# Kernel tuning notes

Hardware: AMD Instinct MI355X
Metric: run time of the kernel (lower is better)

## Reference

```python
import jax, jax.numpy as jnp
import numpy as np

NH = 12   # num_heads
EPS = 1e-6


def _layer_norm(x):
    m = jnp.mean(x, axis=-1, keepdims=True)
    v = jnp.mean((x - m) ** 2, axis=-1, keepdims=True)
    return (x - m) * jax.lax.rsqrt(v + EPS)


def _rms_norm(x, w):
    return x * jax.lax.rsqrt(jnp.mean(x * x, axis=-1, keepdims=True) + EPS) * w


def _rope_cos_sin(f, h, w, head_dim):
    # matches rope_params + calculate_freqs_i: split c=head_dim//2 complex freqs
    # into [c-2*(c//3), c//3, c//3] for the (F,H,W) axes.
    c = head_dim // 2
    inv = 1.0 / (10000.0 ** (np.arange(0, head_dim, 2, dtype=np.float64) / head_dim))
    c1 = c - 2 * (c // 3); c2 = c // 3
    af = np.outer(np.arange(f), inv[:c1])
    ah = np.outer(np.arange(h), inv[c1:c1 + c2])
    aw = np.outer(np.arange(w), inv[c1 + c2:])
    ang = np.concatenate([
        np.broadcast_to(af[:, None, None, :], (f, h, w, c1)),
        np.broadcast_to(ah[None, :, None, :], (f, h, w, c2)),
        np.broadcast_to(aw[None, None, :, :], (f, h, w, c2)),
    ], axis=-1).reshape(f * h * w, c)
    return jnp.asarray(np.cos(ang), jnp.float32), jnp.asarray(np.sin(ang), jnp.float32)


def _apply_rope(x, cos, sin):
    # complex rotation on interleaved pairs; x: [B,L,n,d]
    B, L, n, d = x.shape
    xr = x.reshape(B, L, n, d // 2, 2)
    x0, x1 = xr[..., 0], xr[..., 1]
    co = cos[None, :, None, :]; si = sin[None, :, None, :]
    return jnp.stack([x0 * co - x1 * si, x0 * si + x1 * co], axis=-1).reshape(B, L, n, d)


def _attention(q, k, v):
    scale = 1.0 / jnp.sqrt(jnp.asarray(q.shape[-1], q.dtype))
    s = jnp.einsum('blnd,bmnd->bnlm', q, k) * scale
    return jnp.einsum('bnlm,bmnd->blnd', jax.nn.softmax(s, axis=-1), v)


def _block(x, e, context, mod, sa_wq, sa_bq, sa_wk, sa_bk, sa_wv, sa_bv, sa_wo, sa_bo,
           sa_nq, sa_nk, n3_w, n3_b, ca_wq, ca_bq, ca_wk, ca_bk, ca_wv, ca_bv, ca_wo,
           ca_bo, ca_nq, ca_nk, ffn_w1, ffn_b1, ffn_w2, ffn_b2, f, h, w):
    B, L, C = x.shape
    D = C // NH
    em = mod + e                      # [B,6,C] AdaLN shift/scale/gate params
    cos, sin = _rope_cos_sin(f, h, w, D)
    # --- self-attention with AdaLN modulation + RoPE + qk RMSNorm ---
    xa = _layer_norm(x) * (1.0 + em[:, 1:2]) + em[:, 0:1]
    q = _rms_norm(xa @ sa_wq + sa_bq, sa_nq).reshape(B, L, NH, D)
    k = _rms_norm(xa @ sa_wk + sa_bk, sa_nk).reshape(B, L, NH, D)
    v = (xa @ sa_wv + sa_bv).reshape(B, L, NH, D)
    q = _apply_rope(q, cos, sin)
    k = _apply_rope(k, cos, sin)
    y = _attention(q, k, v).reshape(B, L, C) @ sa_wo + sa_bo
    x = x + y * em[:, 2:3]
    # --- t2v cross-attention (norm3 is affine LayerNorm) ---
    L2 = context.shape[1]
    xc = _layer_norm(x) * n3_w + n3_b
    q = _rms_norm(xc @ ca_wq + ca_bq, ca_nq).reshape(B, L, NH, D)
    k = _rms_norm(context @ ca_wk + ca_bk, ca_nk).reshape(B, L2, NH, D)
    v = (context @ ca_wv + ca_bv).reshape(B, L2, NH, D)
    x = x + (_attention(q, k, v).reshape(B, L, C) @ ca_wo + ca_bo)
    # --- FFN (GELU-tanh) with AdaLN modulation ---
    xf = _layer_norm(x) * (1.0 + em[:, 4:5]) + em[:, 3:4]
    y = jax.nn.gelu(xf @ ffn_w1 + ffn_b1, approximate=True) @ ffn_w2 + ffn_b2
    return x + y * em[:, 5:6]


def setup_inputs() -> dict:
    key = jax.random.key(0)
    ks = jax.random.split(key, 16)
    B, L2, C, FFN = 1, 512, 1536, 8960
    F, H, W = 9, 16, 28
    L = F * H * W  # 4032
    def mk(i, shape, s=0.02):
        return jax.random.normal(ks[i], shape, jnp.float32) * s
    return {
        'x': jax.random.normal(ks[0], (B, L, C), jnp.float32),
        'e': jax.random.normal(ks[1], (B, 6, C), jnp.float32),
        'context': jax.random.normal(ks[2], (B, L2, C), jnp.float32),
        'mod': jax.random.normal(ks[3], (1, 6, C), jnp.float32) / jnp.sqrt(float(C)),
        'sa_wq': mk(4, (C, C)), 'sa_bq': jnp.zeros((C,), jnp.float32),
        'sa_wk': mk(5, (C, C)), 'sa_bk': jnp.zeros((C,), jnp.float32),
        'sa_wv': mk(6, (C, C)), 'sa_bv': jnp.zeros((C,), jnp.float32),
        'sa_wo': mk(7, (C, C)), 'sa_bo': jnp.zeros((C,), jnp.float32),
        'sa_nq': jnp.ones((C,), jnp.float32), 'sa_nk': jnp.ones((C,), jnp.float32),
        'n3_w': jnp.ones((C,), jnp.float32), 'n3_b': jnp.zeros((C,), jnp.float32),
        'ca_wq': mk(8, (C, C)), 'ca_bq': jnp.zeros((C,), jnp.float32),
        'ca_wk': mk(9, (C, C)), 'ca_bk': jnp.zeros((C,), jnp.float32),
        'ca_wv': mk(10, (C, C)), 'ca_bv': jnp.zeros((C,), jnp.float32),
        'ca_wo': mk(11, (C, C)), 'ca_bo': jnp.zeros((C,), jnp.float32),
        'ca_nq': jnp.ones((C,), jnp.float32), 'ca_nk': jnp.ones((C,), jnp.float32),
        'ffn_w1': mk(12, (C, FFN)), 'ffn_b1': jnp.zeros((FFN,), jnp.float32),
        'ffn_w2': mk(13, (FFN, C)), 'ffn_b2': jnp.zeros((C,), jnp.float32),
        'f': F, 'h': H, 'w': W,
    }


def reference(x, e, context, mod, sa_wq, sa_bq, sa_wk, sa_bk, sa_wv, sa_bv, sa_wo,
              sa_bo, sa_nq, sa_nk, n3_w, n3_b, ca_wq, ca_bq, ca_wk, ca_bk, ca_wv,
              ca_bv, ca_wo, ca_bo, ca_nq, ca_nk, ffn_w1, ffn_b1, ffn_w2, ffn_b2,
              f, h, w):
    return _block(x, e, context, mod, sa_wq, sa_bq, sa_wk, sa_bk, sa_wv, sa_bv,
                  sa_wo, sa_bo, sa_nq, sa_nk, n3_w, n3_b, ca_wq, ca_bq, ca_wk,
                  ca_bk, ca_wv, ca_bv, ca_wo, ca_bo, ca_nq, ca_nk, ffn_w1, ffn_b1,
                  ffn_w2, ffn_b2, f, h, w)
```

## Files before the change

### kernel.cpp

```cpp
#include <hip/hip_runtime.h>
#include <math.h>


#define L_SEQ 4032
#define L_PAD 4096
#define C_DIM 1536
#define L_CTX 512
#define FFN_DIM 8960
#define NHEAD 12
#define DHEAD 128

typedef __attribute__((ext_vector_type(8))) short short8;
typedef __attribute__((ext_vector_type(4))) float floatx4;

__device__ inline unsigned short f2bf(float x) {
  unsigned int u = __float_as_uint(x);
  u += 0x7fffu + ((u >> 16) & 1u);
  return (unsigned short)(u >> 16);
}

__device__ inline float2 block_sum2(float2 v) {
  __shared__ float2 red[4];
#pragma unroll
  for (int o = 32; o > 0; o >>= 1) {
    v.x += __shfl_xor(v.x, o, 64);
    v.y += __shfl_xor(v.y, o, 64);
  }
  int wave = threadIdx.x >> 6;
  if ((threadIdx.x & 63) == 0) red[wave] = v;
  __syncthreads();
  float2 t = make_float2(0.f, 0.f);
#pragma unroll
  for (int i = 0; i < 4; ++i) { t.x += red[i].x; t.y += red[i].y; }
  return t;
}

__global__ void add_kernel(float* __restrict__ o, const float* __restrict__ a,
                           const float* __restrict__ b, int n) {
  int i = blockIdx.x * 256 + threadIdx.x;
  if (i < n) o[i] = a[i] + b[i];
}

__global__ void concat3_kernel(float* __restrict__ o, const float* __restrict__ a,
                               const float* __restrict__ b, const float* __restrict__ c) {
  int i = blockIdx.x * 256 + threadIdx.x;
  if (i < C_DIM) {
    o[i] = a[i];
    o[C_DIM + i] = b[i];
    if (c) o[2 * C_DIM + i] = c[i];
  }
}

__global__ void f32_to_bf16_kernel(unsigned short* __restrict__ o,
                                   const float* __restrict__ in, int n) {
  int i = (blockIdx.x * 256 + threadIdx.x) * 4;
  if (i < n) {
    float4 v = *(const float4*)&in[i];
    ushort4 o4 = {f2bf(v.x), f2bf(v.y), f2bf(v.z), f2bf(v.w)};
    *(ushort4*)&o[i] = o4;
  }
}

__global__ __launch_bounds__(256) void transpose_bf16_kernel(
    const float* __restrict__ W, unsigned short* __restrict__ WT, int K, int N) {
  __shared__ float t[32][33];
  int n0 = blockIdx.x * 32, k0 = blockIdx.y * 32;
  int c = threadIdx.x & 31, r0 = threadIdx.x >> 5;
#pragma unroll
  for (int i = 0; i < 4; ++i) {
    int r = r0 + 8 * i;
    t[r][c] = W[(size_t)(k0 + r) * N + n0 + c];
  }
  __syncthreads();
#pragma unroll
  for (int i = 0; i < 4; ++i) {
    int r = r0 + 8 * i;
    WT[(size_t)(n0 + r) * K + k0 + c] = f2bf(t[c][r]);
  }
}

__global__ __launch_bounds__(256) void transpose_v_kernel(
    const float* __restrict__ V, unsigned short* __restrict__ Vt, int stride, int Lk) {
  __shared__ float t[32][33];
  int k0 = blockIdx.x * 32, c0 = blockIdx.y * 32;
  int c = threadIdx.x & 31, r0 = threadIdx.x >> 5;
#pragma unroll
  for (int i = 0; i < 4; ++i) {
    int r = r0 + 8 * i;
    t[r][c] = V[(size_t)(k0 + r) * stride + c0 + c];
  }
  __syncthreads();
#pragma unroll
  for (int i = 0; i < 4; ++i) {
    int r = r0 + 8 * i;
    Vt[(size_t)(c0 + r) * Lk + k0 + c] = f2bf(t[c][r]);
  }
}

__global__ __launch_bounds__(256) void ln_affine_kernel(
    unsigned short* __restrict__ out, const float* __restrict__ in,
    const float* __restrict__ sc, const float* __restrict__ sh, float addOne) {
  int row = blockIdx.x;
  const float* xr = in + (size_t)row * C_DIM;
  float vals[C_DIM / 256];
  float2 p = make_float2(0.f, 0.f);
  int cnt = 0;
  for (int c = threadIdx.x; c < C_DIM; c += 256) {
    float v = xr[c];
    vals[cnt++] = v;
    p.x += v; p.y += v * v;
  }
  float2 t = block_sum2(p);
  float mean = t.x * (1.f / C_DIM);
  float var = t.y * (1.f / C_DIM) - mean * mean;
  float r = rsqrtf(var + 1e-6f);
  cnt = 0;
  for (int c = threadIdx.x; c < C_DIM; c += 256) {
    float xh = (vals[cnt++] - mean) * r;
    out[(size_t)row * C_DIM + c] = f2bf(xh * (addOne + sc[c]) + sh[c]);
  }
}

template <int ROPE>
__global__ __launch_bounds__(256) void rms_post_kernel(
    unsigned short* __restrict__ obf, const float* __restrict__ in,
    const float* __restrict__ w, const float* __restrict__ cosb,
    const float* __restrict__ sinb, int stride, float ps) {
  int row = blockIdx.x;
  const float* xr = in + (size_t)row * stride;
  int c0 = threadIdx.x * 6;
  float v[6];
  *(float2*)&v[0] = *(const float2*)&xr[c0];
  *(float2*)&v[2] = *(const float2*)&xr[c0 + 2];
  *(float2*)&v[4] = *(const float2*)&xr[c0 + 4];
  float s2 = 0.f;
#pragma unroll
  for (int i = 0; i < 6; ++i) s2 += v[i] * v[i];
  float2 t = block_sum2(make_float2(s2, 0.f));
  float r = rsqrtf(t.x * (1.f / C_DIM) + 1e-6f) * ps;
#pragma unroll
  for (int i = 0; i < 6; ++i) v[i] *= r * w[c0 + i];
  if (ROPE) {
#pragma unroll
    for (int i = 0; i < 3; ++i) {
      int c = c0 + 2 * i;
      int j = (c & 127) >> 1;
      float co = cosb[row * 64 + j], si = sinb[row * 64 + j];
      float a = v[2 * i], b = v[2 * i + 1];
      v[2 * i] = a * co - b * si;
      v[2 * i + 1] = a * si + b * co;
    }
  }
  unsigned short* op = obf + (size_t)row * C_DIM + c0;
  ushort2 o01 = {f2bf(v[0]), f2bf(v[1])};
  ushort2 o23 = {f2bf(v[2]), f2bf(v[3])};
  ushort2 o45 = {f2bf(v[4]), f2bf(v[5])};
  *(ushort2*)&op[0] = o01;
  *(ushort2*)&op[2] = o23;
  *(ushort2*)&op[4] = o45;
}

__global__ void rope_tables_kernel(float* __restrict__ cosb, float* __restrict__ sinb) {
  int l = blockIdx.x, j = threadIdx.x;
  int f = l / (16 * 28);
  int rem = l % (16 * 28);
  int hh = rem / 28, ww = rem % 28;
  double inv = pow(10000.0, -(double)(2 * j) / 128.0);
  double pos = (j < 22) ? (double)f : ((j < 43) ? (double)hh : (double)ww);
  double ang = pos * inv;
  cosb[l * 64 + j] = (float)cos(ang);
  sinb[l * 64 + j] = (float)sin(ang);
}

__device__ inline float gelu_tanh(float x) {
  float x3 = x * x * x;
  return 0.5f * x * (1.f + tanhf(0.79788456080286535588f * (x + 0.044715f * x3)));
}

__device__ inline int xcd_remap(int flat, int nwg) {
  int qq = nwg >> 3, rr = nwg & 7;
  int xcd = flat & 7, idx = flat >> 3;
  return (xcd < rr ? xcd * (qq + 1) : rr * (qq + 1) + (xcd - rr) * qq) + idx;
}

template <int EPI>
__global__ __launch_bounds__(256) void mgemm_kernel(
    const unsigned short* __restrict__ A, const unsigned short* __restrict__ BT,
    const float* __restrict__ bias, void* __restrict__ Cout,
    const float* __restrict__ resid, const float* __restrict__ gate,
    int N, int K, int Mlimit) {
  __shared__ short sA[3][4096];
  __shared__ short sB[3][4096];
  const int tid = threadIdx.x;
  const int wv = tid >> 6, lane = tid & 63;
  const int lm = lane & 15, lq = lane >> 4;
  const int wr = wv >> 1, wc = wv & 1;

  const int gx = gridDim.x;
  int flat = xcd_remap(blockIdx.y * gx + blockIdx.x, gx * gridDim.y);
  const int row0 = (flat / gx) * 128, col0 = (flat % gx) * 128;

  floatx4 zero4 = {0.f, 0.f, 0.f, 0.f};
  floatx4 acc[4][4];
#pragma unroll
  for (int i = 0; i < 4; ++i)
#pragma unroll
    for (int j = 0; j < 4; ++j) acc[i][j] = zero4;

  const unsigned short* Abase = A + ((size_t)row0 + lm) * K + lq * 8;
  const unsigned short* Bbase = BT + ((size_t)col0 + lm) * K + lq * 8;

  auto stage = [&](int buf, int k0) {
#pragma unroll
    for (int t = 0; t < 2; ++t) {
      int g = wv * 2 + t;
      __builtin_amdgcn_global_load_lds(
          (const __attribute__((address_space(1))) void*)(Abase + (size_t)(g * 16) * K + k0),
          (__attribute__((address_space(3))) void*)(sA[buf] + g * 512), 16, 0, 0);
      __builtin_amdgcn_global_load_lds(
          (const __attribute__((address_space(1))) void*)(Bbase + (size_t)(g * 16) * K + k0),
          (__attribute__((address_space(3))) void*)(sB[buf] + g * 512), 16, 0, 0);
    }
  };

  stage(0, 0);
  stage(1, 32);
  asm volatile("s_waitcnt vmcnt(4)" ::: "memory");
  __builtin_amdgcn_s_barrier();
  __builtin_amdgcn_sched_barrier(0);

  int cur = 0;
  const int nk = K >> 5;
  for (int t = 0; t < nk; ++t) {
    int b2 = cur + 2; if (b2 >= 3) b2 -= 3;
    const bool more = (t + 2 < nk);
    if (more) stage(b2, (t + 2) << 5);
    const short* sAc = &sA[cur][0];
    const short* sBc = &sB[cur][0];
    short8 af[4], bfv[4];
#pragma unroll
    for (int mt = 0; mt < 4; ++mt)
      af[mt] = *(const short8*)(sAc + (wr * 4 + mt) * 512 + lane * 8);
#pragma unroll
    for (int nt = 0; nt < 4; ++nt)
      bfv[nt] = *(const short8*)(sBc + (wc * 4 + nt) * 512 + lane * 8);
#pragma unroll
    for (int mt = 0; mt < 4; ++mt)
#pragma unroll
      for (int nt = 0; nt < 4; ++nt)
        acc[mt][nt] = __builtin_amdgcn_mfma_f32_16x16x32_bf16(
            af[mt], bfv[nt], acc[mt][nt], 0, 0, 0);
    __builtin_amdgcn_sched_barrier(0);
    if (more) { asm volatile("s_waitcnt vmcnt(4)" ::: "memory"); }
    else      { asm volatile("s_waitcnt vmcnt(0)" ::: "memory"); }
    __builtin_amdgcn_s_barrier();
    __builtin_amdgcn_sched_barrier(0);
    cur = (cur + 1 == 3) ? 0 : cur + 1;
  }

#pragma unroll
  for (int nt = 0; nt < 4; ++nt) {
    int colg = col0 + wc * 64 + nt * 16 + lm;
    float bv = bias[colg];
    float gv = (EPI == 2 && gate) ? gate[colg] : 1.f;
#pragma unroll
    for (int mt = 0; mt < 4; ++mt) {
#pragma unroll
      for (int r = 0; r < 4; ++r) {
        int rowg = row0 + wr * 64 + mt * 16 + lq * 4 + r;
        if (rowg < Mlimit) {
          float v = acc[mt][nt][r] + bv;
          if (EPI == 1) {
            ((unsigned short*)Cout)[(size_t)rowg * N + colg] = f2bf(gelu_tanh(v));
          } else if (EPI == 2) {
            ((float*)Cout)[(size_t)rowg * N + colg] =
                resid[(size_t)rowg * N + colg] + v * gv;
          } else {
            ((float*)Cout)[(size_t)rowg * N + colg] = v;
          }
        }
      }
    }
  }
}

template <int EPI>
__global__ __launch_bounds__(256) void mgemm64_kernel(
    const unsigned short* __restrict__ A, const unsigned short* __restrict__ BT,
    const float* __restrict__ bias, void* __restrict__ Cout,
    const float* __restrict__ resid, const float* __restrict__ gate,
    int N, int K, int Mlimit) {
  __shared__ short sA[3][2048];
  __shared__ short sB[3][4096];
  const int tid = threadIdx.x;
  const int wv = tid >> 6, lane = tid & 63;
  const int lm = lane & 15, lq = lane >> 4;
  const int wc = wv;

  const int gx = gridDim.x;
  int flat = xcd_remap(blockIdx.y * gx + blockIdx.x, gx * gridDim.y);
  const int row0 = (flat / gx) * 64, col0 = (flat % gx) * 128;

  floatx4 zero4 = {0.f, 0.f, 0.f, 0.f};
  floatx4 acc[4][2];
#pragma unroll
  for (int i = 0; i < 4; ++i)
#pragma unroll
    for (int j = 0; j < 2; ++j) acc[i][j] = zero4;

  const unsigned short* Abase = A + ((size_t)row0 + lm) * K + lq * 8;
  const unsigned short* Bbase = BT + ((size_t)col0 + lm) * K + lq * 8;

  auto stage = [&](int buf, int k0) {
    __builtin_amdgcn_global_load_lds(
        (const __attribute__((address_space(1))) void*)(Abase + (size_t)(wv * 16) * K + k0),
        (__attribute__((address_space(3))) void*)(sA[buf] + wv * 512), 16, 0, 0);
#pragma unroll
    for (int t = 0; t < 2; ++t) {
      int g = wv * 2 + t;
      __builtin_amdgcn_global_load_lds(
          (const __attribute__((address_space(1))) void*)(Bbase + (size_t)(g * 16) * K + k0),
          (__attribute__((address_space(3))) void*)(sB[buf] + g * 512), 16, 0, 0);
    }
  };

  stage(0, 0);
  stage(1, 32);
  asm volatile("s_waitcnt vmcnt(3)" ::: "memory");
  __builtin_amdgcn_s_barrier();
  __builtin_amdgcn_sched_barrier(0);

  int cur = 0;
  const int nk = K >> 5;
  for (int t = 0; t < nk; ++t) {
    int b2 = cur + 2; if (b2 >= 3) b2 -= 3;
    const bool more = (t + 2 < nk);
    if (more) stage(b2, (t + 2) << 5);
    const short* sAc = &sA[cur][0];
    const short* sBc = &sB[cur][0];
    short8 af[4], bfv[2];
#pragma unroll
    for (int mt = 0; mt < 4; ++mt)
      af[mt] = *(const short8*)(sAc + mt * 512 + lane * 8);
#pragma unroll
    for (int nt = 0; nt < 2; ++nt)
      bfv[nt] = *(const short8*)(sBc + (wc * 2 + nt) * 512 + lane * 8);
#pragma unroll
    for (int mt = 0; mt < 4; ++mt)
#pragma unroll
      for (int nt = 0; nt < 2; ++nt)
        acc[mt][nt] = __builtin_amdgcn_mfma_f32_16x16x32_bf16(
            af[mt], bfv[nt], acc[mt][nt], 0, 0, 0);
    __builtin_amdgcn_sched_barrier(0);
    if (more) { asm volatile("s_waitcnt vmcnt(3)" ::: "memory"); }
    else      { asm volatile("s_waitcnt vmcnt(0)" ::: "memory"); }
    __builtin_amdgcn_s_barrier();
    __builtin_amdgcn_sched_barrier(0);
    cur = (cur + 1 == 3) ? 0 : cur + 1;
  }

#pragma unroll
  for (int nt = 0; nt < 2; ++nt) {
    int colg = col0 + wc * 32 + nt * 16 + lm;
    float bv = bias[colg];
    float gv = (EPI == 2 && gate) ? gate[colg] : 1.f;
#pragma unroll
    for (int mt = 0; mt < 4; ++mt) {
#pragma unroll
      for (int r = 0; r < 4; ++r) {
        int rowg = row0 + mt * 16 + lq * 4 + r;
        if (rowg < Mlimit) {
          float v = acc[mt][nt][r] + bv;
          if (EPI == 1) {
            ((unsigned short*)Cout)[(size_t)rowg * N + colg] = f2bf(gelu_tanh(v));
          } else if (EPI == 2) {
            ((float*)Cout)[(size_t)rowg * N + colg] =
                resid[(size_t)rowg * N + colg] + v * gv;
          } else {
            ((float*)Cout)[(size_t)rowg * N + colg] = v;
          }
        }
      }
    }
  }
}

__global__ __launch_bounds__(256) void attn_mfma_kernel(
    const unsigned short* __restrict__ Qb, const unsigned short* __restrict__ Kb,
    const unsigned short* __restrict__ Vt, unsigned short* __restrict__ O,
    int Lk) {
  __shared__ short sK[2][4096];
  __shared__ short sV[2][4096];
  __shared__ short sP[4][512];
  const int h = blockIdx.y;
  const int q0 = blockIdx.x * 64;
  const int tid = threadIdx.x;
  const int wv = tid >> 6, lane = tid & 63;
  const int lm = lane & 15, lq = lane >> 4;

  short8 qf[4];
  {
    const unsigned short* qrow =
        Qb + (size_t)(q0 + wv * 16 + lm) * C_DIM + h * DHEAD + lq * 8;
#pragma unroll
    for (int dc = 0; dc < 4; ++dc) qf[dc] = *(const short8*)(qrow + dc * 32);
  }

  floatx4 zero4 = {0.f, 0.f, 0.f, 0.f};
  floatx4 acc[8];
#pragma unroll
  for (int g = 0; g < 8; ++g) acc[g] = zero4;
  float m = -1e30f, l = 0.f;

  auto stageKV = [&](int buf, int k0) {
#pragma unroll
    for (int t = 0; t < 2; ++t) {
      int g = wv * 2 + t;
      int nt_ = g >> 2, dc = g & 3;
      const unsigned short* srck =
          Kb + (size_t)(k0 + nt_ * 16 + lm) * C_DIM + h * DHEAD + dc * 32 + lq * 8;
      __builtin_amdgcn_global_load_lds(
          (const __attribute__((address_space(1))) void*)srck,
          (__attribute__((address_space(3))) void*)(sK[buf] + g * 512), 16, 0, 0);
      const unsigned short* srcv =
          Vt + (size_t)(h * DHEAD + g * 16 + lm) * Lk + k0 + lq * 8;
      __builtin_amdgcn_global_load_lds(
          (const __attribute__((address_space(1))) void*)srcv,
          (__attribute__((address_space(3))) void*)(sV[buf] + g * 512), 16, 0, 0);
    }
  };

  stageKV(0, 0);
  __syncthreads();
  int cur = 0;
  const int nsteps = Lk >> 5;
  for (int t = 0; t < nsteps; ++t) {
    if (t + 1 < nsteps) stageKV(cur ^ 1, (t + 1) << 5);
    const short* sKc = &sK[cur][0];
    const short* sVc = &sV[cur][0];

    floatx4 s0 = zero4, s1 = zero4;
#pragma unroll
    for (int dc = 0; dc < 4; ++dc) {
      short8 kf0 = *(const short8*)(sKc + dc * 512 + lane * 8);
      short8 kf1 = *(const short8*)(sKc + (4 + dc) * 512 + lane * 8);
      s0 = __builtin_amdgcn_mfma_f32_16x16x32_bf16(kf0, qf[dc], s0, 0, 0, 0);
      s1 = __builtin_amdgcn_mfma_f32_16x16x32_bf16(kf1, qf[dc], s1, 0, 0, 0);
    }

    float mx = fmaxf(fmaxf(fmaxf(s0[0], s0[1]), fmaxf(s0[2], s0[3])),
                     fmaxf(fmaxf(s1[0], s1[1]), fmaxf(s1[2], s1[3])));
    mx = fmaxf(mx, __shfl_xor(mx, 16));
    mx = fmaxf(mx, __shfl_xor(mx, 32));
    bool need = mx > m + 11.5f;
    if (__any((int)need)) {
      float mn = fmaxf(m, mx);
      float al = exp2f(m - mn);
      m = mn;
      l *= al;
      float ar[4];
#pragma unroll
      for (int r = 0; r < 4; ++r) ar[r] = __shfl(al, lq * 4 + r);
#pragma unroll
      for (int g = 0; g < 8; ++g)
#pragma unroll
        for (int r = 0; r < 4; ++r) acc[g][r] *= ar[r];
    }
    float rs = 0.f;
    ushort4 pk0, pk1;
#pragma unroll
    for (int r = 0; r < 4; ++r) {
      float p = exp2f(s0[r] - m);
      rs += p;
      ((unsigned short*)&pk0)[r] = f2bf(p);
    }
#pragma unroll
    for (int r = 0; r < 4; ++r) {
      float p = exp2f(s1[r] - m);
      rs += p;
      ((unsigned short*)&pk1)[r] = f2bf(p);
    }
    rs += __shfl_xor(rs, 16);
    rs += __shfl_xor(rs, 32);
    l += rs;
    {
      int baseq = (((lq >> 1) * 16 + lm) << 3) + ((lq & 1) << 2);
      *(ushort4*)&sP[wv][baseq] = pk0;
      *(ushort4*)&sP[wv][baseq + 256] = pk1;
    }
    asm volatile("" ::: "memory");
    short8 pa = *(const short8*)(&sP[wv][lane * 8]);
#pragma unroll
    for (int g = 0; g < 8; ++g) {
      short8 vf = *(const short8*)(sVc + g * 512 + lane * 8);
      acc[g] = __builtin_amdgcn_mfma_f32_16x16x32_bf16(pa, vf, acc[g], 0, 0, 0);
    }
    __syncthreads();
    cur ^= 1;
  }

  float invl[4];
#pragma unroll
  for (int r = 0; r < 4; ++r) invl[r] = 1.f / __shfl(l, lq * 4 + r);
  unsigned short* orow =
      O + (size_t)(q0 + wv * 16 + lq * 4) * C_DIM + h * DHEAD + lm;
#pragma unroll
  for (int g = 0; g < 8; ++g) {
#pragma unroll
    for (int r = 0; r < 4; ++r) {
      orow[(size_t)r * C_DIM + g * 16] = f2bf(acc[g][r] * invl[r]);
    }
  }
}

extern "C" void kernel_launch(void* const* d_in, const int* in_sizes, int n_in,
                              void* d_out, int out_size, void* d_ws, size_t ws_size,
                              hipStream_t stream) {
  const float* x     = (const float*)d_in[0];
  const float* e     = (const float*)d_in[1];
  const float* ctx   = (const float*)d_in[2];
  const float* mod   = (const float*)d_in[3];
  const float* sa_wq = (const float*)d_in[4];
  const float* sa_bq = (const float*)d_in[5];
  const float* sa_wk = (const float*)d_in[6];
  const float* sa_bk = (const float*)d_in[7];
  const float* sa_wv = (const float*)d_in[8];
  const float* sa_bv = (const float*)d_in[9];
  const float* sa_wo = (const float*)d_in[10];
  const float* sa_bo = (const float*)d_in[11];
  const float* sa_nq = (const float*)d_in[12];
  const float* sa_nk = (const float*)d_in[13];
  const float* n3_w  = (const float*)d_in[14];
  const float* n3_b  = (const float*)d_in[15];
  const float* ca_wq = (const float*)d_in[16];
  const float* ca_bq = (const float*)d_in[17];
  const float* ca_wk = (const float*)d_in[18];
  const float* ca_bk = (const float*)d_in[19];
  const float* ca_wv = (const float*)d_in[20];
  const float* ca_bv = (const float*)d_in[21];
  const float* ca_wo = (const float*)d_in[22];
  const float* ca_bo = (const float*)d_in[23];
  const float* ca_nq = (const float*)d_in[24];
  const float* ca_nk = (const float*)d_in[25];
  const float* ffn_w1 = (const float*)d_in[26];
  const float* ffn_b1 = (const float*)d_in[27];
  const float* ffn_w2 = (const float*)d_in[28];
  const float* ffn_b2 = (const float*)d_in[29];
  float* out = (float*)d_out;

  char* wsb = (char*)d_ws;
  auto alloc_f = [&](size_t n) { float* p = (float*)wsb; wsb += ((n * 4 + 255) / 256) * 256; return p; };
  auto alloc_h = [&](size_t n) { unsigned short* p = (unsigned short*)wsb; wsb += ((n * 2 + 255) / 256) * 256; return p; };

  float* em   = alloc_f(6 * C_DIM);
  float* cosb = alloc_f(L_SEQ * 64);
  float* sinb = alloc_f(L_SEQ * 64);
  float* qkv  = alloc_f((size_t)L_SEQ * 3 * C_DIM);
  float* x1b  = alloc_f((size_t)L_SEQ * C_DIM);
  unsigned short* act_bf  = alloc_h((size_t)L_PAD * C_DIM);
  unsigned short* ctx_bf  = alloc_h((size_t)L_CTX * C_DIM);
  unsigned short* wtqkv = alloc_h((size_t)3 * C_DIM * C_DIM);
  unsigned short* wto   = alloc_h((size_t)C_DIM * C_DIM);
  unsigned short* wtcq  = alloc_h((size_t)C_DIM * C_DIM);
  unsigned short* wtckv = alloc_h((size_t)2 * C_DIM * C_DIM);
  unsigned short* wtco  = alloc_h((size_t)C_DIM * C_DIM);
  unsigned short* wt1   = alloc_h((size_t)FFN_DIM * C_DIM);
  unsigned short* wt2   = alloc_h((size_t)C_DIM * FFN_DIM);
  float* qkv_bias = alloc_f(3 * C_DIM);
  float* ckv_bias = alloc_f(2 * C_DIM);
  unsigned short* kbf_x = alloc_h((size_t)L_CTX * C_DIM);
  unsigned short* vtx   = alloc_h((size_t)C_DIM * L_CTX);

  unsigned short* qbf_self = (unsigned short*)x1b;
  unsigned short* kbf_self = ((unsigned short*)x1b) + (size_t)L_SEQ * C_DIM;
  unsigned short* vt_self  = (unsigned short*)out;
  unsigned short* qbf_x    = (unsigned short*)out;
  float* crossq = qkv;
  float* ckv    = qkv + (size_t)L_SEQ * C_DIM;
  unsigned short* ffnh_bf = (unsigned short*)qkv;

  const float qscale = 0.12751649737103347f;

  dim3 gT(C_DIM / 32, C_DIM / 32);
  dim3 gQKV(3 * C_DIM / 128, L_PAD / 128);
  dim3 gGL64(C_DIM / 128, L_PAD / 64);
  dim3 gCKV64(2 * C_DIM / 128, L_CTX / 64);
  dim3 gAtt(L_SEQ / 64, NHEAD);

  transpose_bf16_kernel<<<gT, 256, 0, stream>>>(sa_wq, wtqkv, C_DIM, C_DIM);
  transpose_bf16_kernel<<<gT, 256, 0, stream>>>(sa_wk, wtqkv + (size_t)C_DIM * C_DIM, C_DIM, C_DIM);
  transpose_bf16_kernel<<<gT, 256, 0, stream>>>(sa_wv, wtqkv + (size_t)2 * C_DIM * C_DIM, C_DIM, C_DIM);
  transpose_bf16_kernel<<<gT, 256, 0, stream>>>(sa_wo, wto, C_DIM, C_DIM);
  transpose_bf16_kernel<<<gT, 256, 0, stream>>>(ca_wq, wtcq, C_DIM, C_DIM);
  transpose_bf16_kernel<<<gT, 256, 0, stream>>>(ca_wk, wtckv, C_DIM, C_DIM);
  transpose_bf16_kernel<<<gT, 256, 0, stream>>>(ca_wv, wtckv + (size_t)C_DIM * C_DIM, C_DIM, C_DIM);
  transpose_bf16_kernel<<<gT, 256, 0, stream>>>(ca_wo, wtco, C_DIM, C_DIM);
  transpose_bf16_kernel<<<dim3(FFN_DIM / 32, C_DIM / 32), 256, 0, stream>>>(ffn_w1, wt1, C_DIM, FFN_DIM);
  transpose_bf16_kernel<<<dim3(C_DIM / 32, FFN_DIM / 32), 256, 0, stream>>>(ffn_w2, wt2, FFN_DIM, C_DIM);
  f32_to_bf16_kernel<<<(L_CTX * C_DIM) / 1024, 256, 0, stream>>>(ctx_bf, ctx, L_CTX * C_DIM);
  concat3_kernel<<<6, 256, 0, stream>>>(qkv_bias, sa_bq, sa_bk, sa_bv);
  concat3_kernel<<<6, 256, 0, stream>>>(ckv_bias, ca_bk, ca_bv, nullptr);

  add_kernel<<<(6 * C_DIM + 255) / 256, 256, 0, stream>>>(em, e, mod, 6 * C_DIM);
  rope_tables_kernel<<<L_SEQ, 64, 0, stream>>>(cosb, sinb);

  ln_affine_kernel<<<L_SEQ, 256, 0, stream>>>(act_bf, x, em + C_DIM, em, 1.f);
  mgemm_kernel<0><<<gQKV, 256, 0, stream>>>(act_bf, wtqkv, qkv_bias, qkv,
                                            nullptr, nullptr, 3 * C_DIM, C_DIM, L_SEQ);
  rms_post_kernel<1><<<L_SEQ, 256, 0, stream>>>(qbf_self, qkv, sa_nq, cosb, sinb,
                                                3 * C_DIM, qscale);
  rms_post_kernel<1><<<L_SEQ, 256, 0, stream>>>(kbf_self, qkv + C_DIM, sa_nk, cosb, sinb,
                                                3 * C_DIM, 1.f);
  transpose_v_kernel<<<dim3(L_SEQ / 32, C_DIM / 32), 256, 0, stream>>>(
      qkv + 2 * C_DIM, vt_self, 3 * C_DIM, L_SEQ);
  attn_mfma_kernel<<<gAtt, 256, 0, stream>>>(qbf_self, kbf_self, vt_self, act_bf, L_SEQ);
  mgemm64_kernel<2><<<gGL64, 256, 0, stream>>>(act_bf, wto, sa_bo, x1b,
                                               x, em + 2 * C_DIM, C_DIM, C_DIM, L_SEQ);

  ln_affine_kernel<<<L_SEQ, 256, 0, stream>>>(act_bf, x1b, n3_w, n3_b, 0.f);
  mgemm64_kernel<0><<<gGL64, 256, 0, stream>>>(act_bf, wtcq, ca_bq, crossq,
                                               nullptr, nullptr, C_DIM, C_DIM, L_SEQ);
  rms_post_kernel<0><<<L_SEQ, 256, 0, stream>>>(qbf_x, crossq, ca_nq, cosb, sinb,
                                                C_DIM, qscale);
  mgemm64_kernel<0><<<gCKV64, 256, 0, stream>>>(ctx_bf, wtckv, ckv_bias, ckv,
                                                nullptr, nullptr, 2 * C_DIM, C_DIM, L_CTX);
  rms_post_kernel<0><<<L_CTX, 256, 0, stream>>>(kbf_x, ckv, ca_nk, cosb, sinb,
                                                2 * C_DIM, 1.f);
  transpose_v_kernel<<<dim3(L_CTX / 32, C_DIM / 32), 256, 0, stream>>>(
      ckv + C_DIM, vtx, 2 * C_DIM, L_CTX);
  attn_mfma_kernel<<<gAtt, 256, 0, stream>>>(qbf_x, kbf_x, vtx, act_bf, L_CTX);
  mgemm64_kernel<2><<<gGL64, 256, 0, stream>>>(act_bf, wtco, ca_bo, out,
                                               x1b, nullptr, C_DIM, C_DIM, L_SEQ);

  ln_affine_kernel<<<L_SEQ, 256, 0, stream>>>(act_bf, out, em + 4 * C_DIM, em + 3 * C_DIM, 1.f);
  dim3 g1(FFN_DIM / 128, L_PAD / 128);
  mgemm_kernel<1><<<g1, 256, 0, stream>>>(act_bf, wt1, ffn_b1, ffnh_bf,
                                          nullptr, nullptr, FFN_DIM, C_DIM, L_SEQ);
  dim3 g2(C_DIM / 128, L_PAD / 64);
  mgemm64_kernel<2><<<g2, 256, 0, stream>>>(ffnh_bf, wt2, ffn_b2, out,
                                            out, em + 5 * C_DIM, C_DIM, FFN_DIM, L_SEQ);
}
```

Measured before the change: 1.577 ms.

## Switch GEMMs to K=64 double-buffering, band tile order, bf16 QKV, triple-buffer attention

The GEMM kernels now stage 64-wide K slices into two buffers instead of 32-wide slices into three, and they map tiles in bands of eight rows to improve L2 reuse. The QKV projection writes bf16, so the RMS-norm and V-transpose kernels read half the bytes. The attention kernel's K/V staging moves to a three-buffer pipeline with explicit waitcnt control. The FFN down-projection switches from 64-row to 128-row tiles. Together these target GEMM load latency, memory traffic and attention stalls, at the cost of more LDS per block, which may lower occupancy. Rounding q/k/v to bf16 before normalisation could shift accuracy slightly.

```diff
diff --git a/kernel.cpp b/kernel.cpp
--- a/kernel.cpp
+++ b/kernel.cpp
@@ -18,6 +18,9 @@
   u += 0x7fffu + ((u >> 16) & 1u);
   return (unsigned short)(u >> 16);
 }
+__device__ inline float bf2f(unsigned short u) {
+  return __uint_as_float((unsigned int)u << 16);
+}
 
 __device__ inline float2 block_sum2(float2 v) {
   __shared__ float2 red[4];
@@ -94,6 +97,25 @@
   for (int i = 0; i < 4; ++i) {
     int r = r0 + 8 * i;
     Vt[(size_t)(c0 + r) * Lk + k0 + c] = f2bf(t[c][r]);
+  }
+}
+
+__global__ __launch_bounds__(256) void transpose_v_bf_kernel(
+    const unsigned short* __restrict__ V, unsigned short* __restrict__ Vt,
+    int stride, int Lk) {
+  __shared__ unsigned short t[32][33];
+  int k0 = blockIdx.x * 32, c0 = blockIdx.y * 32;
+  int c = threadIdx.x & 31, r0 = threadIdx.x >> 5;
+#pragma unroll
+  for (int i = 0; i < 4; ++i) {
+    int r = r0 + 8 * i;
+    t[r][c] = V[(size_t)(k0 + r) * stride + c0 + c];
+  }
+  __syncthreads();
+#pragma unroll
+  for (int i = 0; i < 4; ++i) {
+    int r = r0 + 8 * i;
+    Vt[(size_t)(c0 + r) * Lk + k0 + c] = t[c][r];
   }
 }
 
@@ -160,6 +182,45 @@
   *(ushort2*)&op[4] = o45;
 }
 
+template <int ROPE>
+__global__ __launch_bounds__(256) void rms_post_bf_kernel(
+    unsigned short* __restrict__ obf, const unsigned short* __restrict__ in,
+    const float* __restrict__ w, const float* __restrict__ cosb,
+    const float* __restrict__ sinb, int stride, float ps) {
+  int row = blockIdx.x;
+  const unsigned short* xr = in + (size_t)row * stride;
+  int c0 = threadIdx.x * 6;
+  ushort2 a0 = *(const ushort2*)&xr[c0];
+  ushort2 a1 = *(const ushort2*)&xr[c0 + 2];
+  ushort2 a2 = *(const ushort2*)&xr[c0 + 4];
+  float v[6] = {bf2f(a0.x), bf2f(a0.y), bf2f(a1.x), bf2f(a1.y), bf2f(a2.x), bf2f(a2.y)};
+  float s2 = 0.f;
+#pragma unroll
+  for (int i = 0; i < 6; ++i) s2 += v[i] * v[i];
+  float2 t = block_sum2(make_float2(s2, 0.f));
+  float r = rsqrtf(t.x * (1.f / C_DIM) + 1e-6f) * ps;
+#pragma unroll
+  for (int i = 0; i < 6; ++i) v[i] *= r * w[c0 + i];
+  if (ROPE) {
+#pragma unroll
+    for (int i = 0; i < 3; ++i) {
+      int c = c0 + 2 * i;
+      int j = (c & 127) >> 1;
+      float co = cosb[row * 64 + j], si = sinb[row * 64 + j];
+      float a = v[2 * i], b = v[2 * i + 1];
+      v[2 * i] = a * co - b * si;
+      v[2 * i + 1] = a * si + b * co;
+    }
+  }
+  unsigned short* op = obf + (size_t)row * C_DIM + c0;
+  ushort2 o01 = {f2bf(v[0]), f2bf(v[1])};
+  ushort2 o23 = {f2bf(v[2]), f2bf(v[3])};
+  ushort2 o45 = {f2bf(v[4]), f2bf(v[5])};
+  *(ushort2*)&op[0] = o01;
+  *(ushort2*)&op[2] = o23;
+  *(ushort2*)&op[4] = o45;
+}
+
 __global__ void rope_tables_kernel(float* __restrict__ cosb, float* __restrict__ sinb) {
   int l = blockIdx.x, j = threadIdx.x;
   int f = l / (16 * 28);
@@ -183,22 +244,37 @@
   return (xcd < rr ? xcd * (qq + 1) : rr * (qq + 1) + (xcd - rr) * qq) + idx;
 }
 
+__device__ inline void tile_coords(int gx, int gy, int& tx, int& ty) {
+  int nwg = gx * gy;
+  int flat = xcd_remap(blockIdx.y * gx + blockIdx.x, nwg);
+  if ((gy & 7) == 0) {
+    int bandw = gx << 3;
+    int b = flat / bandw;
+    int r = flat - b * bandw;
+    tx = r >> 3;
+    ty = (b << 3) + (r & 7);
+  } else {
+    ty = flat / gx;
+    tx = flat - ty * gx;
+  }
+}
+
 template <int EPI>
-__global__ __launch_bounds__(256) void mgemm_kernel(
+__global__ __launch_bounds__(256) void mgemm_k64_kernel(
     const unsigned short* __restrict__ A, const unsigned short* __restrict__ BT,
     const float* __restrict__ bias, void* __restrict__ Cout,
     const float* __restrict__ resid, const float* __restrict__ gate,
     int N, int K, int Mlimit) {
-  __shared__ short sA[3][4096];
-  __shared__ short sB[3][4096];
+  __shared__ short sA[2][8192];
+  __shared__ short sB[2][8192];
   const int tid = threadIdx.x;
   const int wv = tid >> 6, lane = tid & 63;
   const int lm = lane & 15, lq = lane >> 4;
   const int wr = wv >> 1, wc = wv & 1;
 
-  const int gx = gridDim.x;
-  int flat = xcd_remap(blockIdx.y * gx + blockIdx.x, gx * gridDim.y);
-  const int row0 = (flat / gx) * 128, col0 = (flat % gx) * 128;
+  int tx, ty;
+  tile_coords(gridDim.x, gridDim.y, tx, ty);
+  const int row0 = ty * 128, col0 = tx * 128;
 
   floatx4 zero4 = {0.f, 0.f, 0.f, 0.f};
   floatx4 acc[4][4];
@@ -212,50 +288,52 @@
 
   auto stage = [&](int buf, int k0) {
 #pragma unroll
-    for (int t = 0; t < 2; ++t) {
-      int g = wv * 2 + t;
-      __builtin_amdgcn_global_load_lds(
-          (const __attribute__((address_space(1))) void*)(Abase + (size_t)(g * 16) * K + k0),
-          (__attribute__((address_space(3))) void*)(sA[buf] + g * 512), 16, 0, 0);
-      __builtin_amdgcn_global_load_lds(
-          (const __attribute__((address_space(1))) void*)(Bbase + (size_t)(g * 16) * K + k0),
-          (__attribute__((address_space(3))) void*)(sB[buf] + g * 512), 16, 0, 0);
+    for (int kk = 0; kk < 2; ++kk) {
+#pragma unroll
+      for (int t = 0; t < 2; ++t) {
+        int g = wv * 2 + t;
+        __builtin_amdgcn_global_load_lds(
+            (const __attribute__((address_space(1))) void*)(Abase + (size_t)(g * 16) * K + k0 + kk * 32),
+            (__attribute__((address_space(3))) void*)(sA[buf] + kk * 4096 + g * 512), 16, 0, 0);
+        __builtin_amdgcn_global_load_lds(
+            (const __attribute__((address_space(1))) void*)(Bbase + (size_t)(g * 16) * K + k0 + kk * 32),
+            (__attribute__((address_space(3))) void*)(sB[buf] + kk * 4096 + g * 512), 16, 0, 0);
+      }
     }
   };
 
   stage(0, 0);
-  stage(1, 32);
-  asm volatile("s_waitcnt vmcnt(4)" ::: "memory");
+  asm volatile("s_waitcnt vmcnt(0)" ::: "memory");
   __builtin_amdgcn_s_barrier();
   __builtin_amdgcn_sched_barrier(0);
 
   int cur = 0;
-  const int nk = K >> 5;
+  const int nk = K >> 6;
   for (int t = 0; t < nk; ++t) {
-    int b2 = cur + 2; if (b2 >= 3) b2 -= 3;
-    const bool more = (t + 2 < nk);
-    if (more) stage(b2, (t + 2) << 5);
-    const short* sAc = &sA[cur][0];
-    const short* sBc = &sB[cur][0];
-    short8 af[4], bfv[4];
-#pragma unroll
-    for (int mt = 0; mt < 4; ++mt)
-      af[mt] = *(const short8*)(sAc + (wr * 4 + mt) * 512 + lane * 8);
-#pragma unroll
-    for (int nt = 0; nt < 4; ++nt)
-      bfv[nt] = *(const short8*)(sBc + (wc * 4 + nt) * 512 + lane * 8);
-#pragma unroll
-    for (int mt = 0; mt < 4; ++mt)
+    if (t + 1 < nk) stage(cur ^ 1, (t + 1) << 6);
+#pragma unroll
+    for (int kk = 0; kk < 2; ++kk) {
+      const short* sAc = &sA[cur][kk * 4096];
+      const short* sBc = &sB[cur][kk * 4096];
+      short8 af[4], bfv[4];
+#pragma unroll
+      for (int mt = 0; mt < 4; ++mt)
+        af[mt] = *(const short8*)(sAc + (wr * 4 + mt) * 512 + lane * 8);
 #pragma unroll
       for (int nt = 0; nt < 4; ++nt)
-        acc[mt][nt] = __builtin_amdgcn_mfma_f32_16x16x32_bf16(
-            af[mt], bfv[nt], acc[mt][nt], 0, 0, 0);
+        bfv[nt] = *(const short8*)(sBc + (wc * 4 + nt) * 512 + lane * 8);
+#pragma unroll
+      for (int mt = 0; mt < 4; ++mt)
+#pragma unroll
+        for (int nt = 0; nt < 4; ++nt)
+          acc[mt][nt] = __builtin_amdgcn_mfma_f32_16x16x32_bf16(
+              af[mt], bfv[nt], acc[mt][nt], 0, 0, 0);
+    }
     __builtin_amdgcn_sched_barrier(0);
-    if (more) { asm volatile("s_waitcnt vmcnt(4)" ::: "memory"); }
-    else      { asm volatile("s_waitcnt vmcnt(0)" ::: "memory"); }
+    asm volatile("s_waitcnt vmcnt(0)" ::: "memory");
     __builtin_amdgcn_s_barrier();
     __builtin_amdgcn_sched_barrier(0);
-    cur = (cur + 1 == 3) ? 0 : cur + 1;
+    cur ^= 1;
   }
 
 #pragma unroll
@@ -275,6 +353,8 @@
           } else if (EPI == 2) {
             ((float*)Cout)[(size_t)rowg * N + colg] =
                 resid[(size_t)rowg * N + colg] + v * gv;
+          } else if (EPI == 3) {
+            ((unsigned short*)Cout)[(size_t)rowg * N + colg] = f2bf(v);
           } else {
             ((float*)Cout)[(size_t)rowg * N + colg] = v;
           }
@@ -285,21 +365,21 @@
 }
 
 template <int EPI>
-__global__ __launch_bounds__(256) void mgemm64_kernel(
+__global__ __launch_bounds__(256) void mgemm64_k64_kernel(
     const unsigned short* __restrict__ A, const unsigned short* __restrict__ BT,
     const float* __restrict__ bias, void* __restrict__ Cout,
     const float* __restrict__ resid, const float* __restrict__ gate,
     int N, int K, int Mlimit) {
-  __shared__ short sA[3][2048];
-  __shared__ short sB[3][4096];
+  __shared__ short sA[2][4096];
+  __shared__ short sB[2][8192];
   const int tid = threadIdx.x;
   const int wv = tid >> 6, lane = tid & 63;
   const int lm = lane & 15, lq = lane >> 4;
   const int wc = wv;
 
-  const int gx = gridDim.x;
-  int flat = xcd_remap(blockIdx.y * gx + blockIdx.x, gx * gridDim.y);
-  const int row0 = (flat / gx) * 64, col0 = (flat % gx) * 128;
+  int tx, ty;
+  tile_coords(gridDim.x, gridDim.y, tx, ty);
+  const int row0 = ty * 64, col0 = tx * 128;
 
   floatx4 zero4 = {0.f, 0.f, 0.f, 0.f};
   floatx4 acc[4][2];
@@ -312,51 +392,53 @@
   const unsigned short* Bbase = BT + ((size_t)col0 + lm) * K + lq * 8;
 
   auto stage = [&](int buf, int k0) {
-    __builtin_amdgcn_global_load_lds(
-        (const __attribute__((address_space(1))) void*)(Abase + (size_t)(wv * 16) * K + k0),
-        (__attribute__((address_space(3))) void*)(sA[buf] + wv * 512), 16, 0, 0);
-#pragma unroll
-    for (int t = 0; t < 2; ++t) {
-      int g = wv * 2 + t;
+#pragma unroll
+    for (int kk = 0; kk < 2; ++kk) {
       __builtin_amdgcn_global_load_lds(
-          (const __attribute__((address_space(1))) void*)(Bbase + (size_t)(g * 16) * K + k0),
-          (__attribute__((address_space(3))) void*)(sB[buf] + g * 512), 16, 0, 0);
+          (const __attribute__((address_space(1))) void*)(Abase + (size_t)(wv * 16) * K + k0 + kk * 32),
+          (__attribute__((address_space(3))) void*)(sA[buf] + kk * 2048 + wv * 512), 16, 0, 0);
+#pragma unroll
+      for (int t = 0; t < 2; ++t) {
+        int g = wv * 2 + t;
+        __builtin_amdgcn_global_load_lds(
+            (const __attribute__((address_space(1))) void*)(Bbase + (size_t)(g * 16) * K + k0 + kk * 32),
+            (__attribute__((address_space(3))) void*)(sB[buf] + kk * 4096 + g * 512), 16, 0, 0);
+      }
     }
   };
 
   stage(0, 0);
-  stage(1, 32);
-  asm volatile("s_waitcnt vmcnt(3)" ::: "memory");
+  asm volatile("s_waitcnt vmcnt(0)" ::: "memory");
   __builtin_amdgcn_s_barrier();
   __builtin_amdgcn_sched_barrier(0);
 
   int cur = 0;
-  const int nk = K >> 5;
+  const int nk = K >> 6;
   for (int t = 0; t < nk; ++t) {
-    int b2 = cur + 2; if (b2 >= 3) b2 -= 3;
-    const bool more = (t + 2 < nk);
-    if (more) stage(b2, (t + 2) << 5);
-    const short* sAc = &sA[cur][0];
-    const short* sBc = &sB[cur][0];
-    short8 af[4], bfv[2];
-#pragma unroll
-    for (int mt = 0; mt < 4; ++mt)
-      af[mt] = *(const short8*)(sAc + mt * 512 + lane * 8);
-#pragma unroll
-    for (int nt = 0; nt < 2; ++nt)
-      bfv[nt] = *(const short8*)(sBc + (wc * 2 + nt) * 512 + lane * 8);
-#pragma unroll
-    for (int mt = 0; mt < 4; ++mt)
+    if (t + 1 < nk) stage(cur ^ 1, (t + 1) << 6);
+#pragma unroll
+    for (int kk = 0; kk < 2; ++kk) {
+      const short* sAc = &sA[cur][kk * 2048];
+      const short* sBc = &sB[cur][kk * 4096];
+      short8 af[4], bfv[2];
+#pragma unroll
+      for (int mt = 0; mt < 4; ++mt)
+        af[mt] = *(const short8*)(sAc + mt * 512 + lane * 8);
 #pragma unroll
       for (int nt = 0; nt < 2; ++nt)
-        acc[mt][nt] = __builtin_amdgcn_mfma_f32_16x16x32_bf16(
-            af[mt], bfv[nt], acc[mt][nt], 0, 0, 0);
+        bfv[nt] = *(const short8*)(sBc + (wc * 2 + nt) * 512 + lane * 8);
+#pragma unroll
+      for (int mt = 0; mt < 4; ++mt)
+#pragma unroll
+        for (int nt = 0; nt < 2; ++nt)
+          acc[mt][nt] = __builtin_amdgcn_mfma_f32_16x16x32_bf16(
+              af[mt], bfv[nt], acc[mt][nt], 0, 0, 0);
+    }
     __builtin_amdgcn_sched_barrier(0);
-    if (more) { asm volatile("s_waitcnt vmcnt(3)" ::: "memory"); }
-    else      { asm volatile("s_waitcnt vmcnt(0)" ::: "memory"); }
+    asm volatile("s_waitcnt vmcnt(0)" ::: "memory");
     __builtin_amdgcn_s_barrier();
     __builtin_amdgcn_sched_barrier(0);
-    cur = (cur + 1 == 3) ? 0 : cur + 1;
+    cur ^= 1;
   }
 
 #pragma unroll
@@ -376,6 +458,8 @@
           } else if (EPI == 2) {
             ((float*)Cout)[(size_t)rowg * N + colg] =
                 resid[(size_t)rowg * N + colg] + v * gv;
+          } else if (EPI == 3) {
+            ((unsigned short*)Cout)[(size_t)rowg * N + colg] = f2bf(v);
           } else {
             ((float*)Cout)[(size_t)rowg * N + colg] = v;
           }
@@ -389,8 +473,8 @@
     const unsigned short* __restrict__ Qb, const unsigned short* __restrict__ Kb,
     const unsigned short* __restrict__ Vt, unsigned short* __restrict__ O,
     int Lk) {
-  __shared__ short sK[2][4096];
-  __shared__ short sV[2][4096];
+  __shared__ short sK[3][4096];
+  __shared__ short sV[3][4096];
   __shared__ short sP[4][512];
   const int h = blockIdx.y;
   const int q0 = blockIdx.x * 64;
@@ -431,11 +515,17 @@
   };
 
   stageKV(0, 0);
-  __syncthreads();
+  stageKV(1, 32);
+  asm volatile("s_waitcnt vmcnt(4)" ::: "memory");
+  __builtin_amdgcn_s_barrier();
+  __builtin_amdgcn_sched_barrier(0);
+
   int cur = 0;
   const int nsteps = Lk >> 5;
   for (int t = 0; t < nsteps; ++t) {
-    if (t + 1 < nsteps) stageKV(cur ^ 1, (t + 1) << 5);
+    int b2 = cur + 2; if (b2 >= 3) b2 -= 3;
+    const bool more = (t + 2 < nsteps);
+    if (more) stageKV(b2, (t + 2) << 5);
     const short* sKc = &sK[cur][0];
     const short* sVc = &sV[cur][0];
 
@@ -495,8 +585,12 @@
       short8 vf = *(const short8*)(sVc + g * 512 + lane * 8);
       acc[g] = __builtin_amdgcn_mfma_f32_16x16x32_bf16(pa, vf, acc[g], 0, 0, 0);
     }
-    __syncthreads();
-    cur ^= 1;
+    __builtin_amdgcn_sched_barrier(0);
+    if (more) { asm volatile("s_waitcnt vmcnt(4)" ::: "memory"); }
+    else      { asm volatile("s_waitcnt vmcnt(0)" ::: "memory"); }
+    __builtin_amdgcn_s_barrier();
+    __builtin_amdgcn_sched_barrier(0);
+    cur = (cur + 1 == 3) ? 0 : cur + 1;
   }
 
   float invl[4];
@@ -571,6 +665,7 @@
   unsigned short* kbf_x = alloc_h((size_t)L_CTX * C_DIM);
   unsigned short* vtx   = alloc_h((size_t)C_DIM * L_CTX);
 
+  unsigned short* qkvh     = (unsigned short*)qkv;
   unsigned short* qbf_self = (unsigned short*)x1b;
   unsigned short* kbf_self = ((unsigned short*)x1b) + (size_t)L_SEQ * C_DIM;
   unsigned short* vt_self  = (unsigned short*)out;
@@ -605,38 +700,38 @@
   rope_tables_kernel<<<L_SEQ, 64, 0, stream>>>(cosb, sinb);
 
   ln_affine_kernel<<<L_SEQ, 256, 0, stream>>>(act_bf, x, em + C_DIM, em, 1.f);
-  mgemm_kernel<0><<<gQKV, 256, 0, stream>>>(act_bf, wtqkv, qkv_bias, qkv,
-                                            nullptr, nullptr, 3 * C_DIM, C_DIM, L_SEQ);
-  rms_post_kernel<1><<<L_SEQ, 256, 0, stream>>>(qbf_self, qkv, sa_nq, cosb, sinb,
-                                                3 * C_DIM, qscale);
-  rms_post_kernel<1><<<L_SEQ, 256, 0, stream>>>(kbf_self, qkv + C_DIM, sa_nk, cosb, sinb,
-                                                3 * C_DIM, 1.f);
-  transpose_v_kernel<<<dim3(L_SEQ / 32, C_DIM / 32), 256, 0, stream>>>(
-      qkv + 2 * C_DIM, vt_self, 3 * C_DIM, L_SEQ);
+  mgemm_k64_kernel<3><<<gQKV, 256, 0, stream>>>(act_bf, wtqkv, qkv_bias, qkvh,
+                                                nullptr, nullptr, 3 * C_DIM, C_DIM, L_SEQ);
+  rms_post_bf_kernel<1><<<L_SEQ, 256, 0, stream>>>(qbf_self, qkvh, sa_nq, cosb, sinb,
+                                                   3 * C_DIM, qscale);
+  rms_post_bf_kernel<1><<<L_SEQ, 256, 0, stream>>>(kbf_self, qkvh + C_DIM, sa_nk, cosb, sinb,
+                                                   3 * C_DIM, 1.f);
+  transpose_v_bf_kernel<<<dim3(L_SEQ / 32, C_DIM / 32), 256, 0, stream>>>(
+      qkvh + 2 * C_DIM, vt_self, 3 * C_DIM, L_SEQ);
   attn_mfma_kernel<<<gAtt, 256, 0, stream>>>(qbf_self, kbf_self, vt_self, act_bf, L_SEQ);
-  mgemm64_kernel<2><<<gGL64, 256, 0, stream>>>(act_bf, wto, sa_bo, x1b,
-                                               x, em + 2 * C_DIM, C_DIM, C_DIM, L_SEQ);
+  mgemm64_k64_kernel<2><<<gGL64, 256, 0, stream>>>(act_bf, wto, sa_bo, x1b,
+                                                   x, em + 2 * C_DIM, C_DIM, C_DIM, L_SEQ);
 
   ln_affine_kernel<<<L_SEQ, 256, 0, stream>>>(act_bf, x1b, n3_w, n3_b, 0.f);
-  mgemm64_kernel<0><<<gGL64, 256, 0, stream>>>(act_bf, wtcq, ca_bq, crossq,
-                                               nullptr, nullptr, C_DIM, C_DIM, L_SEQ);
+  mgemm64_k64_kernel<0><<<gGL64, 256, 0, stream>>>(act_bf, wtcq, ca_bq, crossq,
+                                                   nullptr, nullptr, C_DIM, C_DIM, L_SEQ);
   rms_post_kernel<0><<<L_SEQ, 256, 0, stream>>>(qbf_x, crossq, ca_nq, cosb, sinb,
                                                 C_DIM, qscale);
-  mgemm64_kernel<0><<<gCKV64, 256, 0, stream>>>(ctx_bf, wtckv, ckv_bias, ckv,
-                                                nullptr, nullptr, 2 * C_DIM, C_DIM, L_CTX);
+  mgemm64_k64_kernel<0><<<gCKV64, 256, 0, stream>>>(ctx_bf, wtckv, ckv_bias, ckv,
+                                                    nullptr, nullptr, 2 * C_DIM, C_DIM, L_CTX);
   rms_post_kernel<0><<<L_CTX, 256, 0, stream>>>(kbf_x, ckv, ca_nk, cosb, sinb,
                                                 2 * C_DIM, 1.f);
   transpose_v_kernel<<<dim3(L_CTX / 32, C_DIM / 32), 256, 0, stream>>>(
       ckv + C_DIM, vtx, 2 * C_DIM, L_CTX);
   attn_mfma_kernel<<<gAtt, 256, 0, stream>>>(qbf_x, kbf_x, vtx, act_bf, L_CTX);
-  mgemm64_kernel<2><<<gGL64, 256, 0, stream>>>(act_bf, wtco, ca_bo, out,
-                                               x1b, nullptr, C_DIM, C_DIM, L_SEQ);
+  mgemm64_k64_kernel<2><<<gGL64, 256, 0, stream>>>(act_bf, wtco, ca_bo, out,
+                                                   x1b, nullptr, C_DIM, C_DIM, L_SEQ);
 
   ln_affine_kernel<<<L_SEQ, 256, 0, stream>>>(act_bf, out, em + 4 * C_DIM, em + 3 * C_DIM, 1.f);
   dim3 g1(FFN_DIM / 128, L_PAD / 128);
-  mgemm_kernel<1><<<g1, 256, 0, stream>>>(act_bf, wt1, ffn_b1, ffnh_bf,
-                                          nullptr, nullptr, FFN_DIM, C_DIM, L_SEQ);
-  dim3 g2(C_DIM / 128, L_PAD / 64);
-  mgemm64_kernel<2><<<g2, 256, 0, stream>>>(ffnh_bf, wt2, ffn_b2, out,
-                                            out, em + 5 * C_DIM, C_DIM, FFN_DIM, L_SEQ);
-}
+  mgemm_k64_kernel<1><<<g1, 256, 0, stream>>>(act_bf, wt1, ffn_b1, ffnh_bf,
+                                              nullptr, nullptr, FFN_DIM, C_DIM, L_SEQ);
+  dim3 g2(C_DIM / 128, L_PAD / 128);
+  mgemm_k64_kernel<2><<<g2, 256, 0, stream>>>(ffnh_bf, wt2, ffn_b2, out,
+                                              out, em + 5 * C_DIM, C_DIM, FFN_DIM, L_SEQ);
+}
```

New measurement: 1.656 ms. 1.05x slower.
